# Kernel tuning notes

Hardware: AMD Instinct MI355X
Metric: run time of the kernel (lower is better)

Reference implementation:

```python
import jax, jax.numpy as jnp
import numpy as np

NUM_EMBEDDINGS = 1024
EMBEDDING_DIM = 256
COMMITMENT_COST = 0.25
DECAY = 0.99
EPSILON = 1e-5


def setup_inputs() -> dict:
    key = jax.random.key(0)
    k1, k2 = jax.random.split(key)
    B, C, D, H, W = 4, EMBEDDING_DIM, 16, 32, 32
    z = jax.random.normal(k1, (B, C, D, H, W), dtype=jnp.float32)
    bound = 1.0 / (EMBEDDING_DIM ** 0.5)  # nn.init.uniform_(-1/sqrt(d), 1/sqrt(d))
    embed = jax.random.uniform(k2, (NUM_EMBEDDINGS, EMBEDDING_DIM), dtype=jnp.float32,
                               minval=-bound, maxval=bound)
    ema_cluster_size = jnp.zeros((NUM_EMBEDDINGS,), dtype=jnp.float32)
    ema_embed_sum = embed  # buffer initialized as a clone of the embedding weight
    return {"z": z, "embed": embed,
            "ema_cluster_size": ema_cluster_size, "ema_embed_sum": ema_embed_sum}


def reference(z, embed, ema_cluster_size, ema_embed_sum):
    """Training-mode forward of VectorQuantizer (EMA codebook update included).

    Returns (z_q [B,C,D,H,W], vq_loss scalar, indices [B,D,H,W]).
    """
    K, Dm = embed.shape
    B, C, D, H, W = z.shape
    # (B,C,D,H,W) -> (B,D,H,W,C) -> (N, Dm)
    zp = jnp.transpose(z, (0, 2, 3, 4, 1))
    zf = zp.reshape(-1, Dm)

    # squared-distance via expanded cdist: |z|^2 + |e|^2 - 2 z e^T
    dist = (jnp.sum(zf * zf, axis=1, keepdims=True)
            + jnp.sum(embed * embed, axis=1)
            - 2.0 * jnp.matmul(zf, embed.T))  # (N, K)
    idx = jnp.argmin(dist, axis=1)  # (N,)

    # EMA statistics (one-hot matmuls expressed as segment sums)
    batch_cluster_size = jax.ops.segment_sum(jnp.ones_like(idx, dtype=zf.dtype), idx,
                                             num_segments=K)
    batch_embed_sum = jax.ops.segment_sum(zf, idx, num_segments=K)  # (K, Dm)
    new_ema_cs = DECAY * ema_cluster_size + (1.0 - DECAY) * batch_cluster_size
    new_ema_es = DECAY * ema_embed_sum + (1.0 - DECAY) * batch_embed_sum
    n = jnp.sum(new_ema_cs)
    cluster_size = (new_ema_cs + EPSILON) / (n + K * EPSILON) * n
    new_embed = new_ema_es / cluster_size[:, None]  # updated codebook, used for gather

    z_q = new_embed[idx].reshape(zp.shape)  # (B,D,H,W,C)
    vq_loss = COMMITMENT_COST * jnp.mean((zp - jax.lax.stop_gradient(z_q)) ** 2)
    z_q = zp + jax.lax.stop_gradient(z_q - zp)  # straight-through

    indices = idx.reshape(B, D, H, W)
    z_q = jnp.transpose(z_q, (0, 4, 1, 2, 3))  # back to (B,C,D,H,W)
    return z_q, vq_loss, indices
```

## Files before the change

### kernel.cpp

```cpp
#include <hip/hip_runtime.h>
#include <hip/hip_bf16.h>
#include <cfloat>

#define NTOT    65536
#define KCODES  1024
#define DM      256
#define SPAT    16384
#define ZQ_SIZE 16777216

#define WS_ENORM 0
#define WS_CSIZE 1024
#define WS_START 2048
#define WS_LOSSP 3104
#define WS_HIST  11296
#define WS_SORT  273440
#define WS_IDX   338976
#define WS_NEWE  404512

__global__ __launch_bounds__(256) void enorm_kernel(const float* __restrict__ embed,
                                                    float* __restrict__ enorm) {
    int k = blockIdx.x;
    int t = threadIdx.x;
    float v = embed[k * DM + t];
    v *= v;
    #pragma unroll
    for (int m = 32; m > 0; m >>= 1) v += __shfl_xor(v, m);
    __shared__ float sm[4];
    if ((t & 63) == 0) sm[t >> 6] = v;
    __syncthreads();
    if (t == 0) enorm[k] = sm[0] + sm[1] + sm[2] + sm[3];
}

__global__ __launch_bounds__(256, 4) void argmin_kernel(
    const float* __restrict__ z, const float* __restrict__ embed,
    const float* __restrict__ enorm, int* __restrict__ idx_out,
    float* __restrict__ dout) {
    __shared__ float zs[64][68];
    __shared__ float es[64][68];

    const int tid = threadIdx.x;
    const int n0  = blockIdx.x * 64;
    const int b   = n0 >> 14;
    const int s0  = n0 & 16383;
    const int ti  = tid >> 4;
    const int tj  = tid & 15;
    const int sl  = tid & 63;
    const int cg  = tid >> 6;
    const int kg4 = tid >> 4;
    const int cl4 = tid & 15;

    float best[4]  = {FLT_MAX, FLT_MAX, FLT_MAX, FLT_MAX};
    int   bestk[4] = {0, 0, 0, 0};

    for (int k0 = 0; k0 < KCODES; k0 += 64) {
        float acc[4][4] = {};
        for (int c0 = 0; c0 < DM; c0 += 64) {
            __syncthreads();
            {
                const float* zp = z + (size_t)(b * DM + c0 + cg * 16) * SPAT + s0 + sl;
                #pragma unroll
                for (int u = 0; u < 16; ++u)
                    zs[sl][cg * 16 + u] = zp[(size_t)u * SPAT];
            }
            {
                #pragma unroll
                for (int v = 0; v < 4; ++v) {
                    int kk = kg4 + v * 16;
                    float4 val = *(const float4*)&embed[(size_t)(k0 + kk) * DM + c0 + cl4 * 4];
                    *(float4*)&es[kk][cl4 * 4] = val;
                }
            }
            __syncthreads();
            #pragma unroll
            for (int c = 0; c < 64; c += 4) {
                float4 za[4], eb[4];
                #pragma unroll
                for (int i = 0; i < 4; ++i) za[i] = *(const float4*)&zs[ti + i * 16][c];
                #pragma unroll
                for (int j = 0; j < 4; ++j) eb[j] = *(const float4*)&es[tj + j * 16][c];
                #pragma unroll
                for (int i = 0; i < 4; ++i)
                    #pragma unroll
                    for (int j = 0; j < 4; ++j) {
                        acc[i][j] = fmaf(za[i].x, eb[j].x, acc[i][j]);
                        acc[i][j] = fmaf(za[i].y, eb[j].y, acc[i][j]);
                        acc[i][j] = fmaf(za[i].z, eb[j].z, acc[i][j]);
                        acc[i][j] = fmaf(za[i].w, eb[j].w, acc[i][j]);
                    }
            }
        }
        #pragma unroll
        for (int j = 0; j < 4; ++j) {
            int q = k0 + tj + j * 16;
            float en = enorm[q];
            #pragma unroll
            for (int i = 0; i < 4; ++i) {
                float v = fmaf(-2.0f, acc[i][j], en);
                if (v < best[i]) { best[i] = v; bestk[i] = q; }
            }
        }
    }
    #pragma unroll
    for (int i = 0; i < 4; ++i) {
        float bd = best[i];
        int   bk = bestk[i];
        #pragma unroll
        for (int m = 1; m < 16; m <<= 1) {
            float od = __shfl_xor(bd, m);
            int   ok = __shfl_xor(bk, m);
            if (od < bd || (od == bd && ok < bk)) { bd = od; bk = ok; }
        }
        if (tj == 0) {
            int n = n0 + ti + i * 16;
            idx_out[n] = bk;
            dout[ZQ_SIZE + 1 + n] = (float)bk;
        }
    }
}

__global__ __launch_bounds__(256) void transpose_kernel(const float* __restrict__ z,
                                                        float* __restrict__ zt) {
    __shared__ float zs[64][68];
    int bi = blockIdx.x;
    int st = bi & 255, rest = bi >> 8;
    int ct = rest & 3, b = rest >> 2;
    int n0 = b * SPAT + st * 64;
    int c0 = ct * 64;
    int tid = threadIdx.x;
    int sl = tid & 63, cg = tid >> 6;
    {
        const float* zp = z + (size_t)(b * DM + c0 + cg * 16) * SPAT + (st * 64) + sl;
        #pragma unroll
        for (int u = 0; u < 16; ++u)
            zs[sl][cg * 16 + u] = zp[(size_t)u * SPAT];
    }
    __syncthreads();
    int cc = tid & 15, rr = tid >> 4;
    #pragma unroll
    for (int u = 0; u < 4; ++u) {
        int row = rr + u * 16;
        float4 v = *(const float4*)&zs[row][cc * 4];
        *(float4*)&zt[(size_t)(n0 + row) * DM + c0 + cc * 4] = v;
    }
}

__global__ __launch_bounds__(256) void hist_kernel(const int* __restrict__ idx,
                                                   int* __restrict__ hist) {
    __shared__ int lh[KCODES];
    int ch = blockIdx.x, t = threadIdx.x;
    #pragma unroll
    for (int u = 0; u < 4; ++u) lh[t + u * 256] = 0;
    __syncthreads();
    int k = idx[ch * 256 + t];
    atomicAdd(&lh[k], 1);
    __syncthreads();
    #pragma unroll
    for (int u = 0; u < 4; ++u)
        hist[ch * KCODES + t + u * 256] = lh[t + u * 256];
}

__global__ __launch_bounds__(1024) void scan_kernel(
    int* __restrict__ hist, const float* __restrict__ ema_cs,
    int* __restrict__ start, float* __restrict__ csize) {
    int k = threadIdx.x;
    int run = 0;
    for (int ch = 0; ch < 256; ++ch) {
        int t = hist[ch * KCODES + k];
        hist[ch * KCODES + k] = run;
        run += t;
    }
    int lane = k & 63, wv = k >> 6;
    int v = run;
    #pragma unroll
    for (int d = 1; d < 64; d <<= 1) {
        int t = __shfl_up(v, d);
        if (lane >= d) v += t;
    }
    __shared__ int wsum[16];
    if (lane == 63) wsum[wv] = v;
    __syncthreads();
    __shared__ int wpre[16];
    if (k == 0) {
        int s = 0;
        #pragma unroll
        for (int i = 0; i < 16; ++i) { wpre[i] = s; s += wsum[i]; }
    }
    __syncthreads();
    int excl = wpre[wv] + v - run;
    start[k] = excl;
    if (k == 1023) start[1024] = excl + run;
    float ncs = 0.99f * ema_cs[k] + 0.01f * (float)run;
    float r = ncs;
    #pragma unroll
    for (int m = 32; m > 0; m >>= 1) r += __shfl_xor(r, m);
    __shared__ float fs[16];
    if (lane == 0) fs[wv] = r;
    __syncthreads();
    __shared__ float nt;
    if (k == 0) {
        float s = 0.f;
        #pragma unroll
        for (int i = 0; i < 16; ++i) s += fs[i];
        nt = s;
    }
    __syncthreads();
    float n = nt;
    csize[k] = (ncs + 1e-5f) / (n + 1024.0f * 1e-5f) * n;
}

__global__ __launch_bounds__(256) void rank_scatter_kernel(
    const int* __restrict__ idx, const int* __restrict__ hist,
    const int* __restrict__ start, int* __restrict__ sorted) {
    __shared__ int lidx[256];
    int ch = blockIdx.x, t = threadIdx.x;
    int k = idx[ch * 256 + t];
    lidx[t] = k;
    __syncthreads();
    int rank = 0;
    for (int j = 0; j < 255; ++j)
        if (j < t && lidx[j] == k) ++rank;
    sorted[start[k] + hist[ch * KCODES + k] + rank] = ch * 256 + t;
}

__global__ __launch_bounds__(256) void gather_kernel(
    const float* __restrict__ zt, const int* __restrict__ sorted,
    const int* __restrict__ start, const float* __restrict__ ema_es,
    const float* __restrict__ csize, float* __restrict__ newe) {
    int k = blockIdx.x, c = threadIdx.x;
    int s0 = start[k], s1 = start[k + 1];
    float acc = 0.f;
    for (int i = s0; i < s1; ++i) {
        int n = sorted[i];
        acc += zt[(size_t)n * DM + c];
    }
    size_t o = (size_t)k * DM + c;
    newe[o] = (0.99f * ema_es[o] + 0.01f * acc) / csize[k];
}

__global__ __launch_bounds__(256) void output_kernel(
    const float* __restrict__ z, const float* __restrict__ newe,
    const int* __restrict__ idx, float* __restrict__ dout,
    float* __restrict__ lossp) {
    int gid = blockIdx.x * 256 + threadIdx.x;
    float lsum = 0.f;
    #pragma unroll
    for (int it = 0; it < 8; ++it) {
        int o = gid + it * (8192 * 256);
        int s = o & 16383, t2 = o >> 14;
        int c = t2 & 255, b = t2 >> 8;
        int n = (b << 14) + s;
        int k = idx[n];
        float v = newe[(size_t)k * DM + c];
        float zv = z[o];
        dout[o] = v;
        float d = zv - v;
        lsum = fmaf(d, d, lsum);
    }
    #pragma unroll
    for (int m = 32; m > 0; m >>= 1) lsum += __shfl_xor(lsum, m);
    __shared__ float sm[4];
    int t = threadIdx.x;
    if ((t & 63) == 0) sm[t >> 6] = lsum;
    __syncthreads();
    if (t == 0) lossp[blockIdx.x] = sm[0] + sm[1] + sm[2] + sm[3];
}

__global__ __launch_bounds__(256) void loss_final_kernel(const float* __restrict__ lossp,
                                                         float* __restrict__ dout) {
    int t = threadIdx.x;
    float v = 0.f;
    for (int i = t; i < 8192; i += 256) v += lossp[i];
    #pragma unroll
    for (int m = 32; m > 0; m >>= 1) v += __shfl_xor(v, m);
    __shared__ float sm[4];
    if ((t & 63) == 0) sm[t >> 6] = v;
    __syncthreads();
    if (t == 0) dout[ZQ_SIZE] = 0.25f * ((sm[0] + sm[1] + sm[2] + sm[3]) / 16777216.0f);
}

extern "C" void kernel_launch(void* const* d_in, const int* in_sizes, int n_in,
                              void* d_out, int out_size, void* d_ws, size_t ws_size,
                              hipStream_t stream) {
    const float* z      = (const float*)d_in[0];
    const float* embed  = (const float*)d_in[1];
    const float* ema_cs = (const float*)d_in[2];
    const float* ema_es = (const float*)d_in[3];
    float* out = (float*)d_out;
    float* ws  = (float*)d_ws;

    float* enorm = ws + WS_ENORM;
    float* csize = ws + WS_CSIZE;
    int*   start = (int*)(ws + WS_START);
    float* lossp = ws + WS_LOSSP;
    int*   hist  = (int*)(ws + WS_HIST);
    int*   sortd = (int*)(ws + WS_SORT);
    int*   idx   = (int*)(ws + WS_IDX);
    float* newe  = ws + WS_NEWE;
    float* zt    = out;

    enorm_kernel<<<KCODES, 256, 0, stream>>>(embed, enorm);
    argmin_kernel<<<NTOT / 64, 256, 0, stream>>>(z, embed, enorm, idx, out);
    transpose_kernel<<<4096, 256, 0, stream>>>(z, zt);
    hist_kernel<<<256, 256, 0, stream>>>(idx, hist);
    scan_kernel<<<1, 1024, 0, stream>>>(hist, ema_cs, start, csize);
    rank_scatter_kernel<<<256, 256, 0, stream>>>(idx, hist, start, sortd);
    gather_kernel<<<KCODES, 256, 0, stream>>>(zt, sortd, start, ema_es, csize, newe);
    output_kernel<<<8192, 256, 0, stream>>>(z, newe, idx, out, lossp);
    loss_final_kernel<<<1, 256, 0, stream>>>(lossp, out);
}
```

Before: 775.1 us.

## Enlarge argmin code tile, prefetch into registers, fuse z transpose

The argmin GEMM tile grows from 64 to 128 codes per pass, so each thread holds a 4x8 accumulator and the z tile is reloaded half as often. The next z and embed slices are prefetched into registers while the current tile is computed, overlapping global loads with FMAs. The separate transpose kernel is folded into the first four iterations of argmin, which write zt from shared memory and save one full pass over z. In exchange, register and LDS use rise and occupancy drops (launch bounds go from 4 to 3 blocks per CU).

After: 732.2 us. 5.5% less time.

```diff
diff --git a/kernel.cpp b/kernel.cpp
--- a/kernel.cpp
+++ b/kernel.cpp
@@ -31,12 +31,12 @@
     if (t == 0) enorm[k] = sm[0] + sm[1] + sm[2] + sm[3];
 }
 
-__global__ __launch_bounds__(256, 4) void argmin_kernel(
+__global__ __launch_bounds__(256, 3) void argmin_kernel(
     const float* __restrict__ z, const float* __restrict__ embed,
     const float* __restrict__ enorm, int* __restrict__ idx_out,
-    float* __restrict__ dout) {
+    float* __restrict__ dout, float* __restrict__ zt) {
     __shared__ float zs[64][68];
-    __shared__ float es[64][68];
+    __shared__ float es[128][68];
 
     const int tid = threadIdx.x;
     const int n0  = blockIdx.x * 64;
@@ -46,60 +46,95 @@
     const int tj  = tid & 15;
     const int sl  = tid & 63;
     const int cg  = tid >> 6;
-    const int kg4 = tid >> 4;
-    const int cl4 = tid & 15;
+    const int ex  = tid >> 4;
+    const int ec  = (tid & 15) * 4;
 
     float best[4]  = {FLT_MAX, FLT_MAX, FLT_MAX, FLT_MAX};
     int   bestk[4] = {0, 0, 0, 0};
-
-    for (int k0 = 0; k0 < KCODES; k0 += 64) {
-        float acc[4][4] = {};
-        for (int c0 = 0; c0 < DM; c0 += 64) {
-            __syncthreads();
-            {
-                const float* zp = z + (size_t)(b * DM + c0 + cg * 16) * SPAT + s0 + sl;
+    float acc[4][8];
+
+    float  zr[16];
+    float4 er[8];
+
+    {
+        const float* zp = z + (size_t)(b * DM + cg * 16) * SPAT + s0 + sl;
+        #pragma unroll
+        for (int u = 0; u < 16; ++u) zr[u] = zp[(size_t)u * SPAT];
+        #pragma unroll
+        for (int v = 0; v < 8; ++v)
+            er[v] = *(const float4*)&embed[(size_t)(ex + v * 16) * DM + ec];
+    }
+
+    for (int it = 0; it < 32; ++it) {
+        const int c0 = (it & 3) * 64;
+        const int k0 = (it >> 2) * 128;
+
+        __syncthreads();
+        #pragma unroll
+        for (int u = 0; u < 16; ++u) zs[sl][cg * 16 + u] = zr[u];
+        #pragma unroll
+        for (int v = 0; v < 8; ++v) *(float4*)&es[ex + v * 16][ec] = er[v];
+        __syncthreads();
+
+        if (it + 1 < 32) {
+            const int c1 = ((it + 1) & 3) * 64;
+            const int k1 = ((it + 1) >> 2) * 128;
+            const float* zp = z + (size_t)(b * DM + c1 + cg * 16) * SPAT + s0 + sl;
+            #pragma unroll
+            for (int u = 0; u < 16; ++u) zr[u] = zp[(size_t)u * SPAT];
+            #pragma unroll
+            for (int v = 0; v < 8; ++v)
+                er[v] = *(const float4*)&embed[(size_t)(k1 + ex + v * 16) * DM + c1 + ec];
+        }
+
+        if (it < 4) {
+            #pragma unroll
+            for (int u = 0; u < 4; ++u) {
+                int row = (tid >> 4) + u * 16;
+                float4 v4 = *(const float4*)&zs[row][(tid & 15) * 4];
+                *(float4*)&zt[(size_t)(n0 + row) * DM + c0 + (tid & 15) * 4] = v4;
+            }
+        }
+
+        if ((it & 3) == 0) {
+            #pragma unroll
+            for (int i = 0; i < 4; ++i)
                 #pragma unroll
-                for (int u = 0; u < 16; ++u)
-                    zs[sl][cg * 16 + u] = zp[(size_t)u * SPAT];
-            }
-            {
+                for (int j = 0; j < 8; ++j) acc[i][j] = 0.f;
+        }
+
+        #pragma unroll 4
+        for (int c = 0; c < 64; c += 4) {
+            float4 za[4], eb[8];
+            #pragma unroll
+            for (int i = 0; i < 4; ++i) za[i] = *(const float4*)&zs[ti + i * 16][c];
+            #pragma unroll
+            for (int j = 0; j < 8; ++j) eb[j] = *(const float4*)&es[tj + j * 16][c];
+            #pragma unroll
+            for (int i = 0; i < 4; ++i)
                 #pragma unroll
-                for (int v = 0; v < 4; ++v) {
-                    int kk = kg4 + v * 16;
-                    float4 val = *(const float4*)&embed[(size_t)(k0 + kk) * DM + c0 + cl4 * 4];
-                    *(float4*)&es[kk][cl4 * 4] = val;
+                for (int j = 0; j < 8; ++j) {
+                    acc[i][j] = fmaf(za[i].x, eb[j].x, acc[i][j]);
+                    acc[i][j] = fmaf(za[i].y, eb[j].y, acc[i][j]);
+                    acc[i][j] = fmaf(za[i].z, eb[j].z, acc[i][j]);
+                    acc[i][j] = fmaf(za[i].w, eb[j].w, acc[i][j]);
+                }
+        }
+
+        if ((it & 3) == 3) {
+            #pragma unroll
+            for (int j = 0; j < 8; ++j) {
+                int q = k0 + tj + j * 16;
+                float en = enorm[q];
+                #pragma unroll
+                for (int i = 0; i < 4; ++i) {
+                    float v = fmaf(-2.0f, acc[i][j], en);
+                    if (v < best[i]) { best[i] = v; bestk[i] = q; }
                 }
             }
-            __syncthreads();
-            #pragma unroll
-            for (int c = 0; c < 64; c += 4) {
-                float4 za[4], eb[4];
-                #pragma unroll
-                for (int i = 0; i < 4; ++i) za[i] = *(const float4*)&zs[ti + i * 16][c];
-                #pragma unroll
-                for (int j = 0; j < 4; ++j) eb[j] = *(const float4*)&es[tj + j * 16][c];
-                #pragma unroll
-                for (int i = 0; i < 4; ++i)
-                    #pragma unroll
-                    for (int j = 0; j < 4; ++j) {
-                        acc[i][j] = fmaf(za[i].x, eb[j].x, acc[i][j]);
-                        acc[i][j] = fmaf(za[i].y, eb[j].y, acc[i][j]);
-                        acc[i][j] = fmaf(za[i].z, eb[j].z, acc[i][j]);
-                        acc[i][j] = fmaf(za[i].w, eb[j].w, acc[i][j]);
-                    }
-            }
-        }
-        #pragma unroll
-        for (int j = 0; j < 4; ++j) {
-            int q = k0 + tj + j * 16;
-            float en = enorm[q];
-            #pragma unroll
-            for (int i = 0; i < 4; ++i) {
-                float v = fmaf(-2.0f, acc[i][j], en);
-                if (v < best[i]) { best[i] = v; bestk[i] = q; }
-            }
-        }
-    }
+        }
+    }
+
     #pragma unroll
     for (int i = 0; i < 4; ++i) {
         float bd = best[i];
@@ -115,32 +150,6 @@
             idx_out[n] = bk;
             dout[ZQ_SIZE + 1 + n] = (float)bk;
         }
-    }
-}
-
-__global__ __launch_bounds__(256) void transpose_kernel(const float* __restrict__ z,
-                                                        float* __restrict__ zt) {
-    __shared__ float zs[64][68];
-    int bi = blockIdx.x;
-    int st = bi & 255, rest = bi >> 8;
-    int ct = rest & 3, b = rest >> 2;
-    int n0 = b * SPAT + st * 64;
-    int c0 = ct * 64;
-    int tid = threadIdx.x;
-    int sl = tid & 63, cg = tid >> 6;
-    {
-        const float* zp = z + (size_t)(b * DM + c0 + cg * 16) * SPAT + (st * 64) + sl;
-        #pragma unroll
-        for (int u = 0; u < 16; ++u)
-            zs[sl][cg * 16 + u] = zp[(size_t)u * SPAT];
-    }
-    __syncthreads();
-    int cc = tid & 15, rr = tid >> 4;
-    #pragma unroll
-    for (int u = 0; u < 4; ++u) {
-        int row = rr + u * 16;
-        float4 v = *(const float4*)&zs[row][cc * 4];
-        *(float4*)&zt[(size_t)(n0 + row) * DM + c0 + cc * 4] = v;
     }
 }
 
@@ -299,8 +308,7 @@
     float* zt    = out;
 
     enorm_kernel<<<KCODES, 256, 0, stream>>>(embed, enorm);
-    argmin_kernel<<<NTOT / 64, 256, 0, stream>>>(z, embed, enorm, idx, out);
-    transpose_kernel<<<4096, 256, 0, stream>>>(z, zt);
+    argmin_kernel<<<NTOT / 64, 256, 0, stream>>>(z, embed, enorm, idx, out, zt);
     hist_kernel<<<256, 256, 0, stream>>>(idx, hist);
     scan_kernel<<<1, 1024, 0, stream>>>(hist, ema_cs, start, csize);
     rank_scatter_kernel<<<256, 256, 0, stream>>>(idx, hist, start, sortd);
```

## Restructure argmin with resident z tile, async double-buffered codebook, fused transpose

Applied to the files above, without the earlier changes.

The argmin kernel now loads a 32-row by 256-channel z tile into shared memory once per block. It streams codebook tiles with direct global-to-LDS loads into a double buffer, using an XOR swizzle to avoid bank conflicts. The separate transpose kernel is removed, and the argmin kernel writes the transposed z from its resident tile, which saves a second read of z and one launch. In exchange, blocks shrink to 32 rows, so each codebook tile is reused across fewer rows, and occupancy is capped at two blocks per unit.

Measured after the change: 896.2 us. 15.6% more time.

```diff
diff --git a/kernel.cpp b/kernel.cpp
--- a/kernel.cpp
+++ b/kernel.cpp
@@ -17,6 +17,10 @@
 #define WS_IDX   338976
 #define WS_NEWE  404512
 
+#define GLOAD_LDS16(gp, lp) __builtin_amdgcn_global_load_lds( \
+    (const __attribute__((address_space(1))) unsigned int*)(gp), \
+    (__attribute__((address_space(3))) unsigned int*)(lp), 16, 0, 0)
+
 __global__ __launch_bounds__(256) void enorm_kernel(const float* __restrict__ embed,
                                                     float* __restrict__ enorm) {
     int k = blockIdx.x;
@@ -31,77 +35,105 @@
     if (t == 0) enorm[k] = sm[0] + sm[1] + sm[2] + sm[3];
 }
 
-__global__ __launch_bounds__(256, 4) void argmin_kernel(
+__global__ __launch_bounds__(256, 2) void argmin_kernel(
     const float* __restrict__ z, const float* __restrict__ embed,
     const float* __restrict__ enorm, int* __restrict__ idx_out,
-    float* __restrict__ dout) {
-    __shared__ float zs[64][68];
-    __shared__ float es[64][68];
+    float* __restrict__ dout, float* __restrict__ zt) {
+    __shared__ __align__(16) float zs[32][260];
+    __shared__ __align__(16) float es[2][64][64];
 
     const int tid = threadIdx.x;
-    const int n0  = blockIdx.x * 64;
+    const int n0  = blockIdx.x * 32;
     const int b   = n0 >> 14;
     const int s0  = n0 & 16383;
-    const int ti  = tid >> 4;
     const int tj  = tid & 15;
-    const int sl  = tid & 63;
-    const int cg  = tid >> 6;
-    const int kg4 = tid >> 4;
-    const int cl4 = tid & 15;
-
-    float best[4]  = {FLT_MAX, FLT_MAX, FLT_MAX, FLT_MAX};
-    int   bestk[4] = {0, 0, 0, 0};
-
-    for (int k0 = 0; k0 < KCODES; k0 += 64) {
-        float acc[4][4] = {};
-        for (int c0 = 0; c0 < DM; c0 += 64) {
-            __syncthreads();
-            {
-                const float* zp = z + (size_t)(b * DM + c0 + cg * 16) * SPAT + s0 + sl;
+    const int tr  = tid >> 4;
+    const int w   = tid >> 6;
+    const int l   = tid & 63;
+
+    #pragma unroll 8
+    for (int rr = 0; rr < 32; ++rr) {
+        int c = rr * 8 + (tid >> 5);
+        int s = tid & 31;
+        zs[s][c] = z[(size_t)(b * DM + c) * SPAT + s0 + s];
+    }
+    __syncthreads();
+
+    auto stage_es = [&](int s) {
+        const int kk0 = (s >> 2) * 64;
+        const int cc0 = (s & 3) * 64;
+        #pragma unroll
+        for (int v = 0; v < 4; ++v) {
+            int R = w * 16 + v * 4;
+            int r = R + (l >> 4);
+            int gc = cc0 + (((l & 15) ^ (r & 7)) << 2);
+            const float* gp = embed + (size_t)(kk0 + r) * DM + gc;
+            GLOAD_LDS16(gp, &es[s & 1][R][0]);
+        }
+    };
+
+    stage_es(0);
+
+    float best[2]  = {FLT_MAX, FLT_MAX};
+    int   bestk[2] = {0, 0};
+    float acc[2][4];
+
+    for (int st = 0; st < 64; ++st) {
+        const int buf = st & 1;
+        const int c0  = (st & 3) * 64;
+        const int k0  = (st >> 2) * 64;
+
+        asm volatile("s_waitcnt vmcnt(0)" ::: "memory");
+        __builtin_amdgcn_s_barrier();
+        __builtin_amdgcn_sched_barrier(0);
+
+        if (st < 63) stage_es(st + 1);
+
+        if ((st & 3) == 0) {
+            #pragma unroll
+            for (int i = 0; i < 2; ++i)
                 #pragma unroll
-                for (int u = 0; u < 16; ++u)
-                    zs[sl][cg * 16 + u] = zp[(size_t)u * SPAT];
+                for (int j = 0; j < 4; ++j) acc[i][j] = 0.f;
+        }
+
+        #pragma unroll 4
+        for (int c = 0; c < 64; c += 4) {
+            float4 za[2], eb[4];
+            #pragma unroll
+            for (int i = 0; i < 2; ++i)
+                za[i] = *(const float4*)&zs[tr + i * 16][c0 + c];
+            #pragma unroll
+            for (int j = 0; j < 4; ++j) {
+                int kk = tj + j * 16;
+                eb[j] = *(const float4*)&es[buf][kk][((c >> 2) ^ (kk & 7)) << 2];
             }
-            {
+            #pragma unroll
+            for (int i = 0; i < 2; ++i)
                 #pragma unroll
-                for (int v = 0; v < 4; ++v) {
-                    int kk = kg4 + v * 16;
-                    float4 val = *(const float4*)&embed[(size_t)(k0 + kk) * DM + c0 + cl4 * 4];
-                    *(float4*)&es[kk][cl4 * 4] = val;
+                for (int j = 0; j < 4; ++j) {
+                    acc[i][j] = fmaf(za[i].x, eb[j].x, acc[i][j]);
+                    acc[i][j] = fmaf(za[i].y, eb[j].y, acc[i][j]);
+                    acc[i][j] = fmaf(za[i].z, eb[j].z, acc[i][j]);
+                    acc[i][j] = fmaf(za[i].w, eb[j].w, acc[i][j]);
+                }
+        }
+
+        if ((st & 3) == 3) {
+            #pragma unroll
+            for (int j = 0; j < 4; ++j) {
+                int q = k0 + tj + j * 16;
+                float en = enorm[q];
+                #pragma unroll
+                for (int i = 0; i < 2; ++i) {
+                    float v = fmaf(-2.0f, acc[i][j], en);
+                    if (v < best[i]) { best[i] = v; bestk[i] = q; }
                 }
             }
-            __syncthreads();
-            #pragma unroll
-            for (int c = 0; c < 64; c += 4) {
-                float4 za[4], eb[4];
-                #pragma unroll
-                for (int i = 0; i < 4; ++i) za[i] = *(const float4*)&zs[ti + i * 16][c];
-                #pragma unroll
-                for (int j = 0; j < 4; ++j) eb[j] = *(const float4*)&es[tj + j * 16][c];
-                #pragma unroll
-                for (int i = 0; i < 4; ++i)
-                    #pragma unroll
-                    for (int j = 0; j < 4; ++j) {
-                        acc[i][j] = fmaf(za[i].x, eb[j].x, acc[i][j]);
-                        acc[i][j] = fmaf(za[i].y, eb[j].y, acc[i][j]);
-                        acc[i][j] = fmaf(za[i].z, eb[j].z, acc[i][j]);
-                        acc[i][j] = fmaf(za[i].w, eb[j].w, acc[i][j]);
-                    }
-            }
-        }
-        #pragma unroll
-        for (int j = 0; j < 4; ++j) {
-            int q = k0 + tj + j * 16;
-            float en = enorm[q];
-            #pragma unroll
-            for (int i = 0; i < 4; ++i) {
-                float v = fmaf(-2.0f, acc[i][j], en);
-                if (v < best[i]) { best[i] = v; bestk[i] = q; }
-            }
-        }
-    }
-    #pragma unroll
-    for (int i = 0; i < 4; ++i) {
+        }
+    }
+
+    #pragma unroll
+    for (int i = 0; i < 2; ++i) {
         float bd = best[i];
         int   bk = bestk[i];
         #pragma unroll
@@ -111,36 +143,17 @@
             if (od < bd || (od == bd && ok < bk)) { bd = od; bk = ok; }
         }
         if (tj == 0) {
-            int n = n0 + ti + i * 16;
+            int n = n0 + tr + i * 16;
             idx_out[n] = bk;
             dout[ZQ_SIZE + 1 + n] = (float)bk;
         }
     }
-}
-
-__global__ __launch_bounds__(256) void transpose_kernel(const float* __restrict__ z,
-                                                        float* __restrict__ zt) {
-    __shared__ float zs[64][68];
-    int bi = blockIdx.x;
-    int st = bi & 255, rest = bi >> 8;
-    int ct = rest & 3, b = rest >> 2;
-    int n0 = b * SPAT + st * 64;
-    int c0 = ct * 64;
-    int tid = threadIdx.x;
-    int sl = tid & 63, cg = tid >> 6;
-    {
-        const float* zp = z + (size_t)(b * DM + c0 + cg * 16) * SPAT + (st * 64) + sl;
-        #pragma unroll
-        for (int u = 0; u < 16; ++u)
-            zs[sl][cg * 16 + u] = zp[(size_t)u * SPAT];
-    }
-    __syncthreads();
-    int cc = tid & 15, rr = tid >> 4;
-    #pragma unroll
-    for (int u = 0; u < 4; ++u) {
-        int row = rr + u * 16;
-        float4 v = *(const float4*)&zs[row][cc * 4];
-        *(float4*)&zt[(size_t)(n0 + row) * DM + c0 + cc * 4] = v;
+
+    #pragma unroll
+    for (int u = 0; u < 8; ++u) {
+        int r = w * 8 + u;
+        float4 v4 = *(const float4*)&zs[r][l * 4];
+        *(float4*)&zt[(size_t)(n0 + r) * DM + l * 4] = v4;
     }
 }
 
@@ -299,8 +312,7 @@
     float* zt    = out;
 
     enorm_kernel<<<KCODES, 256, 0, stream>>>(embed, enorm);
-    argmin_kernel<<<NTOT / 64, 256, 0, stream>>>(z, embed, enorm, idx, out);
-    transpose_kernel<<<4096, 256, 0, stream>>>(z, zt);
+    argmin_kernel<<<NTOT / 32, 256, 0, stream>>>(z, embed, enorm, idx, out, zt);
     hist_kernel<<<256, 256, 0, stream>>>(idx, hist);
     scan_kernel<<<1, 1024, 0, stream>>>(hist, ema_cs, start, csize);
     rank_scatter_kernel<<<256, 256, 0, stream>>>(idx, hist, start, sortd);
```

## Retile argmin GEMM to 128x128 with double-buffered direct-to-LDS loads

Applied to the files above, without the earlier changes.

The distance/argmin kernel moves from 64x64 tiles with 4x4 per-thread micro-tiles to 128x128 tiles with 8x8 micro-tiles. Shared-memory staging is double buffered and uses global_load_lds to copy global data straight into LDS, with an XOR swizzle on the codebook tile to avoid bank conflicts. The aim is higher arithmetic intensity and overlap of loads with FMAs in the dominant GEMM-like stage. In exchange, register pressure rises (64 accumulators), the occupancy hint drops to 2 blocks, and half as many blocks are launched.

After: 1.001 ms. +29.2%, slower.

```diff
diff --git a/kernel.cpp b/kernel.cpp
--- a/kernel.cpp
+++ b/kernel.cpp
@@ -17,6 +17,10 @@
 #define WS_IDX   338976
 #define WS_NEWE  404512
 
+#define GLOAD_LDS16(gp, lp) __builtin_amdgcn_global_load_lds( \
+    (const __attribute__((address_space(1))) unsigned int*)(gp), \
+    (__attribute__((address_space(3))) unsigned int*)(lp), 16, 0, 0)
+
 __global__ __launch_bounds__(256) void enorm_kernel(const float* __restrict__ embed,
                                                     float* __restrict__ enorm) {
     int k = blockIdx.x;
@@ -31,77 +35,108 @@
     if (t == 0) enorm[k] = sm[0] + sm[1] + sm[2] + sm[3];
 }
 
-__global__ __launch_bounds__(256, 4) void argmin_kernel(
+__global__ __launch_bounds__(256, 2) void argmin_kernel(
     const float* __restrict__ z, const float* __restrict__ embed,
     const float* __restrict__ enorm, int* __restrict__ idx_out,
     float* __restrict__ dout) {
-    __shared__ float zs[64][68];
-    __shared__ float es[64][68];
+    __shared__ __align__(16) float zs[2][32][128];
+    __shared__ __align__(16) float es[2][128][32];
 
     const int tid = threadIdx.x;
-    const int n0  = blockIdx.x * 64;
+    const int n0  = blockIdx.x * 128;
     const int b   = n0 >> 14;
     const int s0  = n0 & 16383;
     const int ti  = tid >> 4;
     const int tj  = tid & 15;
-    const int sl  = tid & 63;
-    const int cg  = tid >> 6;
-    const int kg4 = tid >> 4;
-    const int cl4 = tid & 15;
-
-    float best[4]  = {FLT_MAX, FLT_MAX, FLT_MAX, FLT_MAX};
-    int   bestk[4] = {0, 0, 0, 0};
-
-    for (int k0 = 0; k0 < KCODES; k0 += 64) {
-        float acc[4][4] = {};
-        for (int c0 = 0; c0 < DM; c0 += 64) {
-            __syncthreads();
-            {
-                const float* zp = z + (size_t)(b * DM + c0 + cg * 16) * SPAT + s0 + sl;
+    const int w   = tid >> 6;
+    const int l   = tid & 63;
+
+    auto stage_z = [&](int st, int buf) {
+        const int c0 = (st & 7) * 32;
+        #pragma unroll
+        for (int v = 0; v < 4; ++v) {
+            int colb = w * 8 + v * 2;
+            int cc   = c0 + colb + (l >> 5);
+            const float* gp = z + (size_t)(b * DM + cc) * SPAT + s0 + (l & 31) * 4;
+            GLOAD_LDS16(gp, &zs[buf][colb][0]);
+        }
+    };
+    auto stage_es = [&](int st, int buf) {
+        const int k0 = (st >> 3) * 128;
+        const int c0 = (st & 7) * 32;
+        #pragma unroll
+        for (int v = 0; v < 4; ++v) {
+            int R = w * 32 + v * 8;
+            int r = R + (l >> 3);
+            int gcol = c0 + (((l & 7) ^ (l >> 3)) << 2);
+            const float* gp = embed + (size_t)(k0 + r) * DM + gcol;
+            GLOAD_LDS16(gp, &es[buf][R][0]);
+        }
+    };
+
+    stage_z(0, 0);
+    stage_es(0, 0);
+
+    float best[8], acc[8][8];
+    int   bestk[8];
+    #pragma unroll
+    for (int i = 0; i < 8; ++i) { best[i] = FLT_MAX; bestk[i] = 0; }
+
+    #pragma unroll 1
+    for (int st = 0; st < 64; ++st) {
+        const int buf = st & 1;
+        const int k0  = (st >> 3) * 128;
+
+        __syncthreads();
+
+        if (st < 63) { stage_z(st + 1, buf ^ 1); stage_es(st + 1, buf ^ 1); }
+
+        if ((st & 7) == 0) {
+            #pragma unroll
+            for (int i = 0; i < 8; ++i)
                 #pragma unroll
-                for (int u = 0; u < 16; ++u)
-                    zs[sl][cg * 16 + u] = zp[(size_t)u * SPAT];
-            }
-            {
+                for (int j = 0; j < 8; ++j) acc[i][j] = 0.f;
+        }
+
+        #pragma unroll
+        for (int cs = 0; cs < 32; cs += 4) {
+            float4 eb[8];
+            #pragma unroll
+            for (int j = 0; j < 8; ++j)
+                eb[j] = *(const float4*)&es[buf][tj + j * 16][(((cs >> 2) ^ (tj & 7)) << 2)];
+            float za[8][4];
+            #pragma unroll
+            for (int q = 0; q < 4; ++q)
                 #pragma unroll
-                for (int v = 0; v < 4; ++v) {
-                    int kk = kg4 + v * 16;
-                    float4 val = *(const float4*)&embed[(size_t)(k0 + kk) * DM + c0 + cl4 * 4];
-                    *(float4*)&es[kk][cl4 * 4] = val;
+                for (int i = 0; i < 8; ++i)
+                    za[i][q] = zs[buf][cs + q][ti + i * 16];
+            #pragma unroll
+            for (int i = 0; i < 8; ++i)
+                #pragma unroll
+                for (int j = 0; j < 8; ++j) {
+                    acc[i][j] = fmaf(za[i][0], eb[j].x, acc[i][j]);
+                    acc[i][j] = fmaf(za[i][1], eb[j].y, acc[i][j]);
+                    acc[i][j] = fmaf(za[i][2], eb[j].z, acc[i][j]);
+                    acc[i][j] = fmaf(za[i][3], eb[j].w, acc[i][j]);
+                }
+        }
+
+        if ((st & 7) == 7) {
+            #pragma unroll
+            for (int j = 0; j < 8; ++j) {
+                int q = k0 + tj + j * 16;
+                float en = enorm[q];
+                #pragma unroll
+                for (int i = 0; i < 8; ++i) {
+                    float v = fmaf(-2.0f, acc[i][j], en);
+                    if (v < best[i]) { best[i] = v; bestk[i] = q; }
                 }
             }
-            __syncthreads();
-            #pragma unroll
-            for (int c = 0; c < 64; c += 4) {
-                float4 za[4], eb[4];
-                #pragma unroll
-                for (int i = 0; i < 4; ++i) za[i] = *(const float4*)&zs[ti + i * 16][c];
-                #pragma unroll
-                for (int j = 0; j < 4; ++j) eb[j] = *(const float4*)&es[tj + j * 16][c];
-                #pragma unroll
-                for (int i = 0; i < 4; ++i)
-                    #pragma unroll
-                    for (int j = 0; j < 4; ++j) {
-                        acc[i][j] = fmaf(za[i].x, eb[j].x, acc[i][j]);
-                        acc[i][j] = fmaf(za[i].y, eb[j].y, acc[i][j]);
-                        acc[i][j] = fmaf(za[i].z, eb[j].z, acc[i][j]);
-                        acc[i][j] = fmaf(za[i].w, eb[j].w, acc[i][j]);
-                    }
-            }
-        }
-        #pragma unroll
-        for (int j = 0; j < 4; ++j) {
-            int q = k0 + tj + j * 16;
-            float en = enorm[q];
-            #pragma unroll
-            for (int i = 0; i < 4; ++i) {
-                float v = fmaf(-2.0f, acc[i][j], en);
-                if (v < best[i]) { best[i] = v; bestk[i] = q; }
-            }
-        }
-    }
-    #pragma unroll
-    for (int i = 0; i < 4; ++i) {
+        }
+    }
+
+    #pragma unroll
+    for (int i = 0; i < 8; ++i) {
         float bd = best[i];
         int   bk = bestk[i];
         #pragma unroll
@@ -299,7 +334,7 @@
     float* zt    = out;
 
     enorm_kernel<<<KCODES, 256, 0, stream>>>(embed, enorm);
-    argmin_kernel<<<NTOT / 64, 256, 0, stream>>>(z, embed, enorm, idx, out);
+    argmin_kernel<<<NTOT / 128, 256, 0, stream>>>(z, embed, enorm, idx, out);
     transpose_kernel<<<4096, 256, 0, stream>>>(z, zt);
     hist_kernel<<<256, 256, 0, stream>>>(idx, hist);
     scan_kernel<<<1, 1024, 0, stream>>>(hist, ema_cs, start, csize);
```
